# Performance work log

Hardware: AMD Instinct MI355X
Metric: run time of the kernel (lower is better)

## Reference

```python
import jax, jax.numpy as jnp
import numpy as np

U = 256      # lstm_unit / embedding_fc_unit
V = 100000   # word vocab
WD = 300     # word embedding dim
PD = 64      # pos embedding dim
AD = 64      # action embedding dim
P = 50       # pos vocab
NA = 164     # 4 + 4*dep_num actions
B, T, K, L, S, A, DQ = 64, 128, 4, 128, 64, 64, 32
FORGET_BIAS = 1.0


def lstm_step(x, c, h, W, b):
    z = jnp.concatenate([x, h], -1) @ W + b
    i, j, f, o = jnp.split(z, 4, -1)
    nc = c * jax.nn.sigmoid(f + FORGET_BIAS) + jax.nn.sigmoid(i) * jnp.tanh(j)
    nh = jnp.tanh(nc) * jax.nn.sigmoid(o)
    return nc, nh


def run_lstm(xs, length, W, b):
    # xs: [B, L, D]; TF dynamic_rnn semantics: state frozen and output zeroed past length.
    Bn, Ln, _ = xs.shape
    u = W.shape[1] // 4
    def step(carry, tx):
        c, h = carry
        t, x = tx
        nc, nh = lstm_step(x, c, h, W, b)
        m = (t < length)[:, None]
        return (jnp.where(m, nc, c), jnp.where(m, nh, h)), jnp.where(m, nh, 0.0)
    init = (jnp.zeros((Bn, u), xs.dtype), jnp.zeros((Bn, u), xs.dtype))
    (cf, hf), outs = jax.lax.scan(step, init, (jnp.arange(Ln), jnp.swapaxes(xs, 0, 1)))
    return jnp.swapaxes(outs, 0, 1), (cf, hf)


def reverse_seq(xs, length):
    # tf.reverse_sequence: reverse first `length` steps, leave the rest in place.
    Ln = xs.shape[1]
    t = jnp.arange(Ln)[None, :]
    rev = jnp.where(t < length[:, None], length[:, None] - 1 - t, t)
    return jnp.take_along_axis(xs, rev[:, :, None], axis=1)


def forward(tree_word_id, tree_pos_id, token_word_id, token_pos_id, history_action_id,
            buff_top_id, deque_word_id, deque_pos_id, deque_length, children_order,
            stack_order, stack_length, token_length, history_action_length,
            word_emb, pos_emb, act_emb, wd_W, wd_b, tree_W, tree_b,
            stack0_W, stack0_b, stack1_W, stack1_b,
            fw0_W, fw0_b, bw0_W, bw0_b, fw1_W, fw1_b, bw1_W, bw1_b,
            act0_W, act0_b, act1_W, act1_b, dq0_W, dq0_b, dq1_W, dq1_b,
            fin_W, fin_b):
    Bn = tree_word_id.shape[0]

    def embed(wid, pid):
        e = jnp.concatenate([word_emb[wid], pos_emb[pid]], -1)
        return jax.nn.relu(e @ wd_W + wd_b)

    tree_e = embed(tree_word_id, tree_pos_id)       # [B, T, U]
    token_e = embed(token_word_id, token_pos_id)    # [B, L, U]
    deque_e = embed(deque_word_id, deque_pos_id)    # [B, DQ, U]
    hist_e = act_emb[history_action_id]             # [B, A, AD]

    # ---- tree LSTM over children structure ----
    Tn = tree_e.shape[1]
    Kn = children_order.shape[2]
    batch_col = jnp.arange(Bn)[:, None]
    H0 = jnp.zeros((Tn + 1, Bn, U), tree_e.dtype)
    C0 = jnp.zeros((Tn + 1, Bn, U), tree_e.dtype)

    def body(carry, i):
        H, C = carry
        idx = children_order[:, i]            # [B, K] indices into slots 0..i
        h = H[idx, batch_col]                 # [B, K, U]
        c = C[idx, batch_col]
        x = tree_e[:, i]                      # [B, U]
        hj = h.sum(1)
        ijo = jnp.concatenate([x, hj], -1) @ tree_W[:, :3 * U] + tree_b[:3 * U]
        xk = jnp.broadcast_to(x[:, None, :], (Bn, Kn, x.shape[-1]))
        f = jnp.concatenate([xk, h], -1) @ tree_W[:, 3 * U:] + tree_b[3 * U:]   # [B, K, U]
        ig, jg, og = jnp.split(ijo, 3, -1)
        nc = (c * jax.nn.sigmoid(f + FORGET_BIAS)).sum(1) + jax.nn.sigmoid(ig) * jnp.tanh(jg)
        nh = jnp.tanh(nc) * jax.nn.sigmoid(og)
        return (H.at[i + 1].set(nh), C.at[i + 1].set(nc)), None

    (H, _), _ = jax.lax.scan(body, (H0, C0), jnp.arange(Tn))
    stack_embedded = H[stack_order, batch_col]      # [B, S, U]

    # ---- stack LSTM (2-layer) ----
    o0, _ = run_lstm(stack_embedded, stack_length, stack0_W, stack0_b)
    _, (_, stack_h) = run_lstm(o0, stack_length, stack1_W, stack1_b)

    # ---- buff bi-LSTM (2 stacked bidirectional layers) ----
    fw0_o, _ = run_lstm(token_e, token_length, fw0_W, fw0_b)
    bw0_o, _ = run_lstm(reverse_seq(token_e, token_length), token_length, bw0_W, bw0_b)
    bw0_o = reverse_seq(bw0_o, token_length)
    x1 = jnp.concatenate([fw0_o, bw0_o], -1)
    fw1_o, (_, fw1_h) = run_lstm(x1, token_length, fw1_W, fw1_b)
    bw1_o, _ = run_lstm(reverse_seq(x1, token_length), token_length, bw1_W, bw1_b)
    bw1_o = reverse_seq(bw1_o, token_length)
    bidx = jnp.arange(Bn)
    fw_top = fw1_o[bidx, buff_top_id]
    bw_top = bw1_o[bidx, buff_top_id]
    bw_bottom = bw1_o[bidx, token_length - 1]
    buff_out = jnp.concatenate([fw1_h - fw_top, bw_top - bw_bottom], -1)

    # ---- action LSTM (2-layer) ----
    a0, _ = run_lstm(hist_e, history_action_length, act0_W, act0_b)
    _, (_, act_h) = run_lstm(a0, history_action_length, act1_W, act1_b)

    # ---- deque LSTM (2-layer) ----
    d0, _ = run_lstm(deque_e, deque_length, dq0_W, dq0_b)
    _, (_, dq_h) = run_lstm(d0, deque_length, dq1_W, dq1_b)

    feat = jnp.concatenate([stack_h, buff_out, act_h, dq_h], -1)   # [B, 5U]
    return jax.nn.relu(feat @ fin_W + fin_b)


def setup_inputs():
    key = jax.random.key(0)
    ks = jax.random.split(key, 48)
    r = lambda i, shape: jax.random.normal(ks[i], shape, jnp.float32) * 0.05
    ri = lambda i, shape, hi: jax.random.randint(ks[i], shape, 0, hi)
    inp = {}
    inp['tree_word_id'] = ri(0, (B, T), V)
    inp['tree_pos_id'] = ri(1, (B, T), P)
    inp['token_word_id'] = ri(2, (B, L), V)
    inp['token_pos_id'] = ri(3, (B, L), P)
    inp['history_action_id'] = ri(4, (B, A), NA)
    inp['buff_top_id'] = ri(5, (B,), L // 2)
    inp['deque_word_id'] = ri(6, (B, DQ), V)
    inp['deque_pos_id'] = ri(7, (B, DQ), P)
    inp['deque_length'] = jax.random.randint(ks[8], (B,), 1, DQ + 1)
    co = ri(9, (B, T, K), T)
    # a node may only reference already-computed children slots (<= step index)
    inp['children_order'] = jnp.minimum(co, jnp.arange(T)[None, :, None])
    inp['stack_order'] = ri(10, (B, S), T + 1)
    inp['stack_length'] = jax.random.randint(ks[11], (B,), 1, S + 1)
    inp['token_length'] = jax.random.randint(ks[12], (B,), L // 2, L + 1)
    inp['history_action_length'] = jax.random.randint(ks[13], (B,), 1, A + 1)
    inp['word_emb'] = r(14, (V, WD))
    inp['pos_emb'] = r(15, (P, PD))
    inp['act_emb'] = r(16, (NA, AD))
    inp['wd_W'] = r(17, (WD + PD, U)); inp['wd_b'] = jnp.zeros((U,))
    inp['tree_W'] = r(18, (2 * U, 4 * U)); inp['tree_b'] = jnp.zeros((4 * U,))
    inp['stack0_W'] = r(19, (2 * U, 4 * U)); inp['stack0_b'] = jnp.zeros((4 * U,))
    inp['stack1_W'] = r(20, (2 * U, 4 * U)); inp['stack1_b'] = jnp.zeros((4 * U,))
    inp['fw0_W'] = r(21, (2 * U, 4 * U)); inp['fw0_b'] = jnp.zeros((4 * U,))
    inp['bw0_W'] = r(22, (2 * U, 4 * U)); inp['bw0_b'] = jnp.zeros((4 * U,))
    inp['fw1_W'] = r(23, (3 * U, 4 * U)); inp['fw1_b'] = jnp.zeros((4 * U,))
    inp['bw1_W'] = r(24, (3 * U, 4 * U)); inp['bw1_b'] = jnp.zeros((4 * U,))
    inp['act0_W'] = r(25, (AD + U, 4 * U)); inp['act0_b'] = jnp.zeros((4 * U,))
    inp['act1_W'] = r(26, (2 * U, 4 * U)); inp['act1_b'] = jnp.zeros((4 * U,))
    inp['dq0_W'] = r(27, (2 * U, 4 * U)); inp['dq0_b'] = jnp.zeros((4 * U,))
    inp['dq1_W'] = r(28, (2 * U, 4 * U)); inp['dq1_b'] = jnp.zeros((4 * U,))
    inp['fin_W'] = r(29, (5 * U, NA)); inp['fin_b'] = jnp.zeros((NA,))
    return inp


def reference(tree_word_id, tree_pos_id, token_word_id, token_pos_id, history_action_id,
              buff_top_id, deque_word_id, deque_pos_id, deque_length, children_order,
              stack_order, stack_length, token_length, history_action_length,
              word_emb, pos_emb, act_emb, wd_W, wd_b, tree_W, tree_b,
              stack0_W, stack0_b, stack1_W, stack1_b,
              fw0_W, fw0_b, bw0_W, bw0_b, fw1_W, fw1_b, bw1_W, bw1_b,
              act0_W, act0_b, act1_W, act1_b, dq0_W, dq0_b, dq1_W, dq1_b,
              fin_W, fin_b):
    return forward(tree_word_id, tree_pos_id, token_word_id, token_pos_id, history_action_id,
                   buff_top_id, deque_word_id, deque_pos_id, deque_length, children_order,
                   stack_order, stack_length, token_length, history_action_length,
                   word_emb, pos_emb, act_emb, wd_W, wd_b, tree_W, tree_b,
                   stack0_W, stack0_b, stack1_W, stack1_b,
                   fw0_W, fw0_b, bw0_W, bw0_b, fw1_W, fw1_b, bw1_W, bw1_b,
                   act0_W, act0_b, act1_W, act1_b, dq0_W, dq0_b, dq1_W, dq1_b,
                   fin_W, fin_b)
```

## Files before the change

kernel.cpp:

```cpp
#include <hip/hip_runtime.h>
#include <hip/hip_bf16.h>
#include <hip/hip_fp16.h>
#include <cstdint>

#define BB   64
#define TT   128
#define KK   4
#define LL   128
#define SS   64
#define AA   64
#define DQN  32
#define UU   256
#define NAOUT 164
#define WDIM 300
#define PDIM 64
#define ADIM 64

#define OFF_TREE 0
#define OFF_S0   512
#define OFF_S1   1024
#define OFF_FW0  1536
#define OFF_BW0  2048
#define OFF_FW1  2560
#define OFF_BW1  3328
// ... 7 lines not shown
#define PKH_BW0  768
#define PKH_FW1  1024
#define PKH_BW1  1280
#define PKH_S0   1536
#define PKH_S1   1792
#define PKH_ACT0 2048
#define PKH_ACT1 2304
#define PKH_DQ0  2560
#define PKH_DQ1  2816
#define PK_ROWS_B 3072

typedef unsigned short ushort_t;
typedef unsigned int   uint_t;

__device__ __forceinline__ float bf2f(ushort_t s) {
    return __uint_as_float(((uint_t)s) << 16);
}
__device__ __forceinline__ ushort_t f2bf(float x) {
    __hip_bfloat16 h = __float2bfloat16(x);
    return *reinterpret_cast<ushort_t*>(&h);
}
__device__ __forceinline__ float sigm(float x) { return 1.0f / (1.0f + expf(-x)); }

__device__ __forceinline__ uint_t pack2h(float a, float b) {
    __half2 h = __floats2half2_rn(a, b);
    return *reinterpret_cast<uint_t*>(&h);
}
__device__ __forceinline__ float2 unp2h(uint_t v) {
    __half2 h = *reinterpret_cast<__half2*>(&v);
    return __half22float2(h);
}

template<bool F32>
__device__ __forceinline__ float ld1(const void* p_, size_t i) {
    if constexpr (F32) return reinterpret_cast<const float*>(p_)[i];
    else               return bf2f(reinterpret_cast<const ushort_t*>(p_)[i]);
}

struct P {
    const int *tree_word_id, *tree_pos_id, *token_word_id, *token_pos_id, *history_action_id,
              *buff_top_id, *deque_word_id, *deque_pos_id, *deque_length, *children_order,
              *stack_order, *stack_length, *token_length, *history_action_length;
    const void *word_emb, *pos_emb, *act_emb, *wd_W, *wd_b, *tree_W, *tree_b,
        *stack0_W, *stack0_b, *stack1_W, *stack1_b, *fw0_W, *fw0_b, *bw0_W, *bw0_b,
        *fw1_W, *fw1_b, *bw1_W, *bw1_b, *act0_W, *act0_b, *act1_W, *act1_b,
        *dq0_W, *dq0_b, *dq1_W, *dq1_b, *fin_W, *fin_b;
    int* flag;
    float *stack_h, *fw1_h, *fw_top, *bw_top, *bw_bottom, *act_h, *dq_h;
    float *tree_e;
    ushort_t *token_e, *deque_e, *x1;
    float *H, *C;
    float *a0_seq, *d0_seq, *s0_seq;
    uint2 *zxA, *zxB, *zxC, *zxD, *zxS;
    float4* pkf;
};

__global__ void detect_kernel(const uint_t* w, int* flag) {
    __shared__ int cnt;
    if (threadIdx.x == 0) cnt = 0;
    __syncthreads();
    int local = 0;
    for (int i = threadIdx.x; i < 256; i += 64) {
        uint_t lo = w[i] & 0xFFFFu;
        uint_t e  = (lo >> 7) & 0xFFu;
        if (lo == 0u || (e >= 0x6Cu && e <= 0x7Fu)) local++;
    }
    atomicAdd(&cnt, local);
    __syncthreads();
    if (threadIdx.x == 0) flag[0] = (cnt >= 200) ? 0 : 1;
}

__global__ void sentinel_kernel(void* out, float v) {
    if (threadIdx.x == 0) {
        reinterpret_cast<float*>(out)[0] = v;
        reinterpret_cast<__hip_bfloat16*>(out)[2] = __float2bfloat16(v);
    }
}

__global__ __launch_bounds__(256) void pack_fb_kernel(P p) {
    const bool f32 = (p.flag[0] == 1);
    const int rg = blockIdx.x;
    const int u  = threadIdx.x;
    const void* src; int r;
    if      (rg < 512)  { src = p.tree_W;   r = rg; }
    else if (rg < 1024) { src = p.stack0_W; r = rg - 512; }
    else if (rg < 1536) { src = p.stack1_W; r = rg - 1024; }
    else if (rg < 2048) { src = p.fw0_W;    r = rg - 1536; }
    else if (rg < 2560) { src = p.bw0_W;    r = rg - 2048; }
    else if (rg < 3328) { src = p.fw1_W;    r = rg - 2560; }
    else if (rg < 4096) { src = p.bw1_W;    r = rg - 3328; }
    else if (rg < 4416) { src = p.act0_W;   r = rg - 4096; }
    else if (rg < 4928) { src = p.act1_W;   r = rg - 4416; }
    else if (rg < 5440) { src = p.dq0_W;    r = rg - 4928; }
    else                { src = p.dq1_W;    r = rg - 5440; }
    const size_t ro = (size_t)r * 1024;
    float4 v;
    if (f32) {
        const float* s = reinterpret_cast<const float*>(src) + ro;
        v = make_float4(s[u], s[256 + u], s[512 + u], s[768 + u]);
    } else {
        const ushort_t* s = reinterpret_cast<const ushort_t*>(src) + ro;
        v = make_float4(bf2f(s[u]), bf2f(s[256 + u]), bf2f(s[512 + u]), bf2f(s[768 + u]));
    }
    p.pkf[(size_t)rg * 256 + u] = v;
}

// ... 158 lines not shown
                #pragma unroll
                for (int j = 0; j < 4; ++j) {
                    const float4 wv = w[4 * q + j];
                    zi = fmaf(xv[j], wv.x, zi);
                    zj = fmaf(xv[j], wv.y, zj);
                    zo = fmaf(xv[j], wv.z, zo);
                    fx = fmaf(xv[j], wv.w, fx);
                }
            }
        }
        float f0 = 0.f, f1 = 0.f, f2 = 0.f, f3 = 0.f;
        for (int r0 = 0; r0 < 256; r0 += 16) {
            float4 w[16];
            #pragma unroll
            for (int k = 0; k < 16; ++k) w[k] = Wh[(size_t)(r0 + k) * 256];
            __builtin_amdgcn_sched_barrier(0);
            #pragma unroll
            for (int q = 0; q < 4; ++q) {
                const int r = r0 + 4 * q;
                const float4 hj4 = *reinterpret_cast<const float4*>(s_hj + r);
                const float4 a0  = *reinterpret_cast<const float4*>(s_hk + r);
                const float4 a1  = *reinterpret_cast<const float4*>(s_hk + 256 + r);
                const float4 a2  = *reinterpret_cast<const float4*>(s_hk + 512 + r);
                const float4 a3  = *reinterpret_cast<const float4*>(s_hk + 768 + r);
                const float hjv[4] = {hj4.x, hj4.y, hj4.z, hj4.w};
                const float k0[4]  = {a0.x, a0.y, a0.z, a0.w};
                const float k1[4]  = {a1.x, a1.y, a1.z, a1.w};
                const float k2[4]  = {a2.x, a2.y, a2.z, a2.w};
                const float k3[4]  = {a3.x, a3.y, a3.z, a3.w};
                #pragma unroll
                for (int j = 0; j < 4; ++j) {
                    const float4 wv = w[4 * q + j];
                    zi = fmaf(hjv[j], wv.x, zi);
                    zj = fmaf(hjv[j], wv.y, zj);
                    zo = fmaf(hjv[j], wv.z, zo);
                    f0 = fmaf(k0[j], wv.w, f0);
                    f1 = fmaf(k1[j], wv.w, f1);
                    f2 = fmaf(k2[j], wv.w, f2);
                    f3 = fmaf(k3[j], wv.w, f3);
                }
            }
        }
        const float fsum = c0 * sigm(fx + f0) + c1 * sigm(fx + f1)
                         + c2 * sigm(fx + f2) + c3 * sigm(fx + f3);
        const float nc = fsum + sigm(zi) * tanhf(zj);
        const float nh = tanhf(nc) * sigm(zo);
        __syncthreads();
        H[((size_t)(i + 1) * BB + b) * UU + u] = nh;
        C[((size_t)(i + 1) * BB + b) * UU + u] = nc;
    }
}

template<bool F32>
__device__ void run_token_l0_f4(int b, const P& p, float* smem, bool is_bw) {
    const int u = threadIdx.x;
    float* s_xh = smem;
    const int len = p.token_length[b];
    const float4* __restrict__ Wp = p.pkf + (size_t)(is_bw ? OFF_BW0 : OFF_FW0) * 256 + u;
    const float4 bz = load_bias4<F32>(is_bw ? p.bw0_b : p.fw0_b, u);

    float c0 = 0.f;
    s_xh[256 + u] = 0.f;
    for (int t = 0; t < len; ++t) {
        const int row = is_bw ? (len - 1 - t) : t;
        s_xh[u] = bf2f(p.token_e[((size_t)b * LL + row) * UU + u]);
        __syncthreads();
        const float nh = lstm_step_f4<512>(Wp, bz, s_xh, c0);
        p.x1[((size_t)b * LL + row) * 512 + (is_bw ? 256 : 0) + u] = f2bf(nh);
        __syncthreads();
        s_xh[256 + u] = nh;
    }
}

template<bool F32>
__device__ void run_act_dq_f4(int b, const P& p, float* smem) {
    const int u = threadIdx.x;
    float* s_xh0 = smem;
    float* s_xh1 = smem + 512;

    {
        const int len = p.history_action_length[b];
        const float4* __restrict__ W0 = p.pkf + (size_t)OFF_ACT0 * 256 + u;
        const float4* __restrict__ W1 = p.pkf + (size_t)OFF_ACT1 * 256 + u;
        const float4 bz0 = load_bias4<F32>(p.act0_b, u);
        const float4 bz1 = load_bias4<F32>(p.act1_b, u);
        float ca0 = 0.f, ca1 = 0.f, h1last = 0.f;
        s_xh0[ADIM + u] = 0.f;
        s_xh1[256 + u]  = 0.f;
        for (int t = 0; t < len; ++t) {
            const int aid = p.history_action_id[b * AA + t];
            if (u < ADIM) s_xh0[u] = ld1<F32>(p.act_emb, (size_t)aid * ADIM + u);
            __syncthreads();
            const float nh0 = lstm_step_f4<320>(W0, bz0, s_xh0, ca0);
            __syncthreads();
            s_xh0[ADIM + u] = nh0;
            s_xh1[u]        = nh0;
            __syncthreads();
            const float nh1 = lstm_step_f4<512>(W1, bz1, s_xh1, ca1);
            __syncthreads();
            s_xh1[256 + u] = nh1;
            h1last = nh1;
        }
        p.act_h[b * UU + u] = h1last;
    }
    __syncthreads();
    {
// ... 113 lines not shown
    } else {
        if (chain == 0)      run_stack_f4<false>(b, p, smem);
        else if (chain == 1) run_token_l1_f4<false>(b, p, smem, false);
        else                 run_token_l1_f4<false>(b, p, smem, true);
    }
}

template<bool F32, int R>
__device__ void xpre_compute(const void* __restrict__ W, const void* __restrict__ bias,
                             uint2* __restrict__ zx, int n0,
                             const float* __restrict__ s_xf, const ushort_t* __restrict__ s_xb) {
    const int u = threadIdx.x;
    const float4 bz = load_bias4<F32>(bias, u);
    for (int c = 0; c < 32; c += 8) {
        float4 acc[8];
        #pragma unroll
        for (int n = 0; n < 8; ++n) acc[n] = bz;
        for (int r0 = 0; r0 < R; r0 += 8) {
            float4 w[8];
            #pragma unroll
            for (int k = 0; k < 8; ++k) {
                const size_t ro = (size_t)(r0 + k) * 1024;
                w[k] = make_float4(ld1<F32>(W, ro + u),
                                   ld1<F32>(W, ro + 256 + u),
                                   ld1<F32>(W, ro + 512 + u),
                                   ld1<F32>(W, ro + 768 + u));
            }
            #pragma unroll
            for (int n = 0; n < 8; ++n) {
                float xv[8];
                #pragma unroll
                for (int k = 0; k < 8; ++k)
                    xv[k] = (R == 512) ? bf2f(s_xb[(size_t)(c + n) * 512 + r0 + k])
                                       : s_xf[(size_t)(c + n) * R + r0 + k];
                #pragma unroll
                for (int k = 0; k < 8; ++k) {
                    acc[n].x = fmaf(xv[k], w[k].x, acc[n].x);
                    acc[n].y = fmaf(xv[k], w[k].y, acc[n].y);
                    acc[n].z = fmaf(xv[k], w[k].z, acc[n].z);
                    acc[n].w = fmaf(xv[k], w[k].w, acc[n].w);
                }
            }
        }
        #pragma unroll
        for (int n = 0; n < 8; ++n) {
            uint2 v;
            v.x = pack2h(acc[n].x, acc[n].y);
            v.y = pack2h(acc[n].z, acc[n].w);
            zx[(size_t)(n0 + c + n) * 256 + u] = v;
        }
    }
}

template<bool F32, int STAGE>
__device__ void xpre_impl(const P& p, char* s_raw) {
    float*    s_xf = reinterpret_cast<float*>(s_raw);
    ushort_t* s_xb = reinterpret_cast<ushort_t*>(s_raw);
    const int blk = blockIdx.x;
    const int tid = threadIdx.x;

    const void* W; const void* bias; uint2* zx; int R; int kind; int n0;
    if (STAGE == 0) {
        if (blk < 256)      { W=p.fw0_W;  bias=p.fw0_b;  zx=p.zxA; R=256; kind=0; n0=blk*32; }
        else if (blk < 512) { W=p.bw0_W;  bias=p.bw0_b;  zx=p.zxB; R=256; kind=0; n0=(blk-256)*32; }
        else if (blk < 640) { W=p.act0_W; bias=p.act0_b; zx=p.zxC; R=64;  kind=3; n0=(blk-512)*32; }
        else                { W=p.dq0_W;  bias=p.dq0_b;  zx=p.zxD; R=256; kind=1; n0=(blk-640)*32; }
    } else if (STAGE == 1) {
        if (blk < 256)      { W=p.fw1_W;    bias=p.fw1_b;    zx=p.zxA; R=512; kind=2; n0=blk*32; }
        else if (blk < 512) { W=p.bw1_W;    bias=p.bw1_b;    zx=p.zxB; R=512; kind=2; n0=(blk-256)*32; }
        else if (blk < 640) { W=p.stack0_W; bias=p.stack0_b; zx=p.zxS; R=256; kind=4; n0=(blk-512)*32; }
        else if (blk < 768) { W=p.act1_W;   bias=p.act1_b;   zx=p.zxC; R=256; kind=5; n0=(blk-640)*32; }
        else                { W=p.dq1_W;    bias=p.dq1_b;    zx=p.zxD; R=256; kind=6; n0=(blk-768)*32; }
    } else {
        W=p.stack1_W; bias=p.stack1_b; zx=p.zxS; R=256; kind=7; n0=blk*32;
    }

    if (kind == 0 || kind == 1) {
        const ushort_t* src = (kind == 0 ? p.token_e : p.deque_e) + (size_t)n0 * 256;
        for (int i = tid; i < 32 * 256; i += 256) s_xf[i] = bf2f(src[i]);
    } else if (kind == 2) {
        const ushort_t* src = p.x1 + (size_t)n0 * 512;
        for (int i = tid; i < 32 * 512; i += 256) s_xb[i] = src[i];
    } else if (kind == 3) {
        const int b = n0 >> 6, t0 = n0 & 63;
        for (int i = tid; i < 32 * 64; i += 256) {
            const int t = t0 + (i >> 6), r = i & 63;
            int aid = p.history_action_id[b * AA + t];
            aid = aid < 0 ? 0 : (aid > NAOUT - 1 ? NAOUT - 1 : aid);
            s_xf[i] = ld1<F32>(p.act_emb, (size_t)aid * ADIM + r);
        }
    } else if (kind == 4) {
        const int b = n0 >> 6, t0 = n0 & 63;
        for (int i = tid; i < 32 * 256; i += 256) {
            const int t = t0 + (i >> 8), r = i & 255;
            int so = p.stack_order[b * SS + t];
            so = so < 0 ? 0 : (so > TT ? TT : so);
            s_xf[i] = p.H[((size_t)so * BB + b) * UU + r];
        }
    } else {
        const float* src = (kind == 5 ? p.a0_seq : kind == 6 ? p.d0_seq : p.s0_seq)
                         + (size_t)n0 * 256;
        for (int i = tid; i < 32 * 256; i += 256) s_xf[i] = src[i];
    }
    __syncthreads();

    if (R == 512)      xpre_compute<F32, 512>(W, bias, zx, n0, s_xf, s_xb);
    else if (R == 256) xpre_compute<F32, 256>(W, bias, zx, n0, s_xf, s_xb);
    else               xpre_compute<F32, 64 >(W, bias, zx, n0, s_xf, s_xb);
}

__global__ __launch_bounds__(256) void xpre0_kernel(P p) {
    __shared__ __align__(16) char s_raw[32768];
    if (p.flag[0] == 1) xpre_impl<true, 0>(p, s_raw);
    else                xpre_impl<false, 0>(p, s_raw);
}
__global__ __launch_bounds__(256) void xpre1_kernel(P p) {
    __shared__ __align__(16) char s_raw[32768];
    if (p.flag[0] == 1) xpre_impl<true, 1>(p, s_raw);
    else                xpre_impl<false, 1>(p, s_raw);
}
__global__ __launch_bounds__(256) void xpre2_kernel(P p) {
    __shared__ __align__(16) char s_raw[32768];
    if (p.flag[0] == 1) xpre_impl<true, 2>(p, s_raw);
    else                xpre_impl<false, 2>(p, s_raw);
}

template<bool F32>
__device__ void p1_impl(const P& p, float* smem) {
    const int chain = blockIdx.x >> 6;
    const int b     = blockIdx.x & 63;
    if (chain == 0) { run_tree_f4<F32>(b, p, smem); return; }

    const int u = threadIdx.x;
    float* s_h = smem;
    float c = 0.f;
    s_h[u] = 0.f;
    __syncthreads();

    if (chain == 1 || chain == 2) {
        const bool bw = (chain == 2);
        const int len = p.token_length[b];
        const float4* __restrict__ Wh = p.pkf + (size_t)(bw ? PKH_BW0 : PKH_FW0) * 256 + u;
        const uint2* zx = bw ? p.zxB : p.zxA;
        for (int t = 0; t < len; ++t) {
            const int row = bw ? (len - 1 - t) : t;
            const float4 bz = zx_load(zx, (size_t)b * LL + row, u);
            const float nh = lstm_step_f4<256>(Wh, bz, s_h, c);
            p.x1[((size_t)b * LL + row) * 512 + (bw ? 256 : 0) + u] = f2bf(nh);
            __syncthreads();
            s_h[u] = nh;
            __syncthreads();
        }
    } else if (chain == 3) {
        const int len = p.history_action_length[b];
        const float4* __restrict__ Wh = p.pkf + (size_t)PKH_ACT0 * 256 + u;
        for (int t = 0; t < len; ++t) {
            const float4 bz = zx_load(p.zxC, (size_t)b * AA + t, u);
            const float nh = lstm_step_f4<256>(Wh, bz, s_h, c);
            p.a0_seq[((size_t)b * AA + t) * UU + u] = nh;
            __syncthreads();
            s_h[u] = nh;
            __syncthreads();
        }
    } else {
        const int len = p.deque_length[b];
        const float4* __restrict__ Wh = p.pkf + (size_t)PKH_DQ0 * 256 + u;
        for (int t = 0; t < len; ++t) {
            const float4 bz = zx_load(p.zxD, (size_t)b * DQN + t, u);
            const float nh = lstm_step_f4<256>(Wh, bz, s_h, c);
            p.d0_seq[((size_t)b * DQN + t) * UU + u] = nh;
            __syncthreads();
            s_h[u] = nh;
            __syncthreads();
        }
    }
}

__global__ __launch_bounds__(256) void p1_kernel(P p) {
    __shared__ __align__(16) float smem[1536];
    if (p.flag[0] == 1) p1_impl<true>(p, smem);
    else                p1_impl<false>(p, smem);
}

template<bool F32>
__device__ void p2_impl(const P& p, float* smem) {
    const int chain = blockIdx.x >> 6;
    const int b     = blockIdx.x & 63;
    const int u = threadIdx.x;
    float* s_h = smem;
    float c = 0.f;
    s_h[u] = 0.f;
    __syncthreads();

    if (chain == 0) {
        const int len  = p.token_length[b];
        const int btop = p.buff_top_id[b];
        const float4* __restrict__ Wh = p.pkf + (size_t)PKH_FW1 * 256 + u;
        float hlast = 0.f;
        for (int t = 0; t < len; ++t) {
            const float4 bz = zx_load(p.zxA, (size_t)b * LL + t, u);
            const float nh = lstm_step_f4<256>(Wh, bz, s_h, c);
            if (t == btop) p.fw_top[b * UU + u] = nh;
            __syncthreads();
            s_h[u] = nh;
            __syncthreads();
            hlast = nh;
        }
        p.fw1_h[b * UU + u] = hlast;
    } else if (chain == 1) {
        const int len  = p.token_length[b];
        const int btop = p.buff_top_id[b];
        const float4* __restrict__ Wh = p.pkf + (size_t)PKH_BW1 * 256 + u;
        for (int t = 0; t < len; ++t) {
            const int row = len - 1 - t;
            const float4 bz = zx_load(p.zxB, (size_t)b * LL + row, u);
            const float nh = lstm_step_f4<256>(Wh, bz, s_h, c);
            if (t == 0)              p.bw_bottom[b * UU + u] = nh;
            if (t == len - 1 - btop) p.bw_top[b * UU + u]    = nh;
            __syncthreads();
            s_h[u] = nh;
            __syncthreads();
        }
    } else if (chain == 2) {
        const int len = p.stack_length[b];
        const float4* __restrict__ Wh = p.pkf + (size_t)PKH_S0 * 256 + u;
        for (int t = 0; t < len; ++t) {
            const float4 bz = zx_load(p.zxS, (size_t)b * SS + t, u);
            const float nh = lstm_step_f4<256>(Wh, bz, s_h, c);
            p.s0_seq[((size_t)b * SS + t) * UU + u] = nh;
            __syncthreads();
            s_h[u] = nh;
            __syncthreads();
        }
    } else if (chain == 3) {
        const int len = p.history_action_length[b];
        const float4* __restrict__ Wh = p.pkf + (size_t)PKH_ACT1 * 256 + u;
        float hlast = 0.f;
        for (int t = 0; t < len; ++t) {
            const float4 bz = zx_load(p.zxC, (size_t)b * AA + t, u);
            const float nh = lstm_step_f4<256>(Wh, bz, s_h, c);
            __syncthreads();
            s_h[u] = nh;
            __syncthreads();
            hlast = nh;
        }
        p.act_h[b * UU + u] = hlast;
    } else {
        const int len = p.deque_length[b];
        const float4* __restrict__ Wh = p.pkf + (size_t)PKH_DQ1 * 256 + u;
        float hlast = 0.f;
        for (int t = 0; t < len; ++t) {
            const float4 bz = zx_load(p.zxD, (size_t)b * DQN + t, u);
            const float nh = lstm_step_f4<256>(Wh, bz, s_h, c);
            __syncthreads();
            s_h[u] = nh;
            __syncthreads();
            hlast = nh;
        }
        p.dq_h[b * UU + u] = hlast;
    }
}

__global__ __launch_bounds__(256) void p2_kernel(P p) {
    __shared__ __align__(16) float smem[256];
    if (p.flag[0] == 1) p2_impl<true>(p, smem);
    else                p2_impl<false>(p, smem);
}

template<bool F32>
__device__ void p3_impl(const P& p, float* smem) {
    const int b = blockIdx.x;
    const int u = threadIdx.x;
    float* s_h = smem;
    float c = 0.f;
    s_h[u] = 0.f;
    __syncthreads();
    const int len = p.stack_length[b];
    const float4* __restrict__ Wh = p.pkf + (size_t)PKH_S1 * 256 + u;
    float hlast = 0.f;
    for (int t = 0; t < len; ++t) {
        const float4 bz = zx_load(p.zxS, (size_t)b * SS + t, u);
        const float nh = lstm_step_f4<256>(Wh, bz, s_h, c);
        __syncthreads();
        s_h[u] = nh;
        __syncthreads();
        hlast = nh;
    }
    p.stack_h[b * UU + u] = hlast;
}

__global__ __launch_bounds__(256) void p3_kernel(P p) {
    __shared__ __align__(16) float smem[256];
    if (p.flag[0] == 1) p3_impl<true>(p, smem);
    else                p3_impl<false>(p, smem);
}

template<bool F32>
__device__ __forceinline__ void st_out(void* out, int i, float v) {
    if constexpr (F32) reinterpret_cast<float*>(out)[i] = v;
    else               reinterpret_cast<__hip_bfloat16*>(out)[i] = __float2bfloat16(v);
}

template<bool F32>
__device__ void final_impl(const P& p, void* out, float* s_f) {
    const int b = blockIdx.x;
    const int u = threadIdx.x;
    s_f[u]        = p.stack_h[b * UU + u];
    s_f[256 + u]  = p.fw1_h[b * UU + u] - p.fw_top[b * UU + u];
    s_f[512 + u]  = p.bw_top[b * UU + u] - p.bw_bottom[b * UU + u];
    s_f[768 + u]  = p.act_h[b * UU + u];
    s_f[1024 + u] = p.dq_h[b * UU + u];
    __syncthreads();
    if (u < NAOUT) {
        float acc = ld1<F32>(p.fin_b, u);
        for (int r = 0; r < 1280; ++r)
            acc = fmaf(s_f[r], ld1<F32>(p.fin_W, (size_t)r * NAOUT + u), acc);
        acc = fmaxf(acc, 0.f);
        st_out<F32>(out, b * NAOUT + u, acc);
    }
    if (b == 0 && u == 0) {
        const uint_t POIS = 0xAAAAAAAAu;
        const uint_t* te = reinterpret_cast<const uint_t*>(p.tree_e);
        const uint_t* x1 = reinterpret_cast<const uint_t*>(p.x1);
        const uint_t* sh = reinterpret_cast<const uint_t*>(p.stack_h);
        bool te_p = true, x1_p = true;
        for (int i = 0; i < 8; ++i) { te_p &= (te[i] == POIS); x1_p &= (x1[i] == POIS); }
        bool sh_p = (sh[0] == POIS) && (sh[1] == POIS);
        float sent = 0.f;
        if (te_p)      sent = 3000.f;
        else if (x1_p) sent = 4000.f;
        else if (sh_p) sent = 5000.f;
        else if (*reinterpret_cast<const uint_t*>(p.flag) == POIS) sent = 6000.f;
        if (sent > 0.f) st_out<F32>(out, 0, sent);
    }
}

__global__ __launch_bounds__(256) void final_kernel(P p, void* out) {
// ... 36 lines not shown
    p.wd_b     = d_in[18];
    p.tree_W   = d_in[19];
    p.tree_b   = d_in[20];
    p.stack0_W = d_in[21];
    p.stack0_b = d_in[22];
    p.stack1_W = d_in[23];
    p.stack1_b = d_in[24];
    p.fw0_W    = d_in[25];
    p.fw0_b    = d_in[26];
    p.bw0_W    = d_in[27];
    p.bw0_b    = d_in[28];
    p.fw1_W    = d_in[29];
    p.fw1_b    = d_in[30];
    p.bw1_W    = d_in[31];
    p.bw1_b    = d_in[32];
    p.act0_W   = d_in[33];
    p.act0_b   = d_in[34];
    p.act1_W   = d_in[35];
    p.act1_b   = d_in[36];
    p.dq0_W    = d_in[37];
    p.dq0_b    = d_in[38];
    p.dq1_W    = d_in[39];
    p.dq1_b    = d_in[40];
    p.fin_W    = d_in[41];
    p.fin_b    = d_in[42];

    char* base = (char*)d_ws;

    size_t off = 0;
    p.flag = (int*)(base + off);           off += 256;
    p.stack_h   = (float*)(base + off);    off += (size_t)BB * UU * 4;
    p.fw1_h     = (float*)(base + off);    off += (size_t)BB * UU * 4;
    p.fw_top    = (float*)(base + off);    off += (size_t)BB * UU * 4;
    p.bw_top    = (float*)(base + off);    off += (size_t)BB * UU * 4;
    p.bw_bottom = (float*)(base + off);    off += (size_t)BB * UU * 4;
    p.act_h     = (float*)(base + off);    off += (size_t)BB * UU * 4;
    p.dq_h      = (float*)(base + off);    off += (size_t)BB * UU * 4;
    p.tree_e  = (float*)(base + off);      off += (size_t)BB * TT * UU * 4;
    p.token_e = (ushort_t*)(base + off);   off += (size_t)BB * LL * UU * 2;
    p.deque_e = (ushort_t*)(base + off);   off += (size_t)BB * DQN * UU * 2;
    p.x1      = (ushort_t*)(base + off);   off += (size_t)BB * LL * 512 * 2;
    p.a0_seq  = (float*)(base + off);      off += (size_t)BB * AA * UU * 4;
    p.d0_seq  = (float*)(base + off);      off += (size_t)BB * DQN * UU * 4;
    p.s0_seq  = (float*)(base + off);      off += (size_t)BB * SS * UU * 4;
    p.H       = (float*)(base + off);      off += (size_t)(TT + 1) * BB * UU * 4;
    p.C       = (float*)(base + off);      off += (size_t)(TT + 1) * BB * UU * 4;
    p.zxA     = (uint2*)(base + off);      off += (size_t)BB * LL * UU * 8;
    p.zxB     = (uint2*)(base + off);      off += (size_t)BB * LL * UU * 8;
    p.zxC     = (uint2*)(base + off);      off += (size_t)BB * AA * UU * 8;
    p.zxD     = (uint2*)(base + off);      off += (size_t)BB * DQN * UU * 8;
    p.zxS     = (uint2*)(base + off);      off += (size_t)BB * SS * UU * 8;
    p.pkf     = (float4*)(base + off);     off += (size_t)PK_ROWS_B * 256 * 16;
    const size_t planB_size = off;

    if (ws_size >= planB_size) {
        detect_kernel<<<1, 64, 0, stream>>>((const uint_t*)d_in[14], p.flag);
        pack_h_kernel<<<dim3(PK_ROWS_B), dim3(256), 0, stream>>>(p);
        embed_kernel<<<dim3(BB * TT + BB * LL + BB * DQN), dim3(256), 0, stream>>>(p);
        xpre0_kernel<<<dim3(704), dim3(256), 0, stream>>>(p);
        p1_kernel<<<dim3(5 * BB), dim3(256), 0, stream>>>(p);
        xpre1_kernel<<<dim3(832), dim3(256), 0, stream>>>(p);
        p2_kernel<<<dim3(5 * BB), dim3(256), 0, stream>>>(p);
        xpre2_kernel<<<dim3(128), dim3(256), 0, stream>>>(p);
        p3_kernel<<<dim3(BB), dim3(256), 0, stream>>>(p);
        final_kernel<<<dim3(BB), dim3(256), 0, stream>>>(p, d_out);
        return;
    }

    off = 0;
    p.flag = (int*)(base + off);           off += 16;
    p.stack_h   = (float*)(base + off);    off += (size_t)BB * UU * 4;
    p.fw1_h     = (float*)(base + off);    off += (size_t)BB * UU * 4;
    p.fw_top    = (float*)(base + off);    off += (size_t)BB * UU * 4;
    p.bw_top    = (float*)(base + off);    off += (size_t)BB * UU * 4;
    p.bw_bottom = (float*)(base + off);    off += (size_t)BB * UU * 4;
    p.act_h     = (float*)(base + off);    off += (size_t)BB * UU * 4;
    p.dq_h      = (float*)(base + off);    off += (size_t)BB * UU * 4;
    p.tree_e  = (float*)(base + off);      off += (size_t)BB * TT * UU * 4;
    p.token_e = (ushort_t*)(base + off);   off += (size_t)BB * LL * UU * 2;
    p.deque_e = (ushort_t*)(base + off);   off += (size_t)BB * DQN * UU * 2;
    p.x1      = (ushort_t*)(base + off);   off += (size_t)BB * LL * 512 * 2;
    p.H       = (float*)(base + off);      off += (size_t)(TT + 1) * BB * UU * 4;
    p.C       = (float*)(base + off);      off += (size_t)(TT + 1) * BB * UU * 4;
    p.pkf     = (float4*)(base + off);     off += (size_t)PK_ROWS_FB * 256 * 16;
    p.a0_seq = p.d0_seq = p.s0_seq = (float*)base;
    p.zxA = p.zxB = p.zxC = p.zxD = p.zxS = (uint2*)base;

    if (ws_size < off) {
        sentinel_kernel<<<1, 64, 0, stream>>>(d_out, 7000.f + (float)(ws_size >> 20));
        return;
    }

    detect_kernel<<<1, 64, 0, stream>>>((const uint_t*)d_in[14], p.flag);
    pack_fb_kernel<<<dim3(PK_ROWS_FB), dim3(256), 0, stream>>>(p);
    embed_kernel<<<dim3(BB * TT + BB * LL + BB * DQN), dim3(256), 0, stream>>>(p);
    phase1_fb_kernel<<<dim3(4 * BB), dim3(256), 0, stream>>>(p);
    phase2_fb_kernel<<<dim3(3 * BB), dim3(256), 0, stream>>>(p);
    final_kernel<<<dim3(BB), dim3(256), 0, stream>>>(p, d_out);
}
```

Baseline: 6.336 ms.

## Precompute tree input projections and interleave recurrent chains across CUs

Adds a tree-LSTM input-projection stage to the batched pre-GEMM kernel, writing fp32 float4 gates into a new workspace buffer. The tree recurrence then only does the hidden-state matmul per step, which shortens the serial critical path. The recurrent phases are also remapped so that long chains (tree, token, stack) are spread across the block index with short chains interleaved, which is meant to balance load across CUs. The cost is a larger workspace requirement, an extra 32MB buffer, and idle blocks that exit early.

```diff
diff --git a/kernel.cpp b/kernel.cpp
--- a/kernel.cpp
+++ b/kernel.cpp
@@ -83,6 +83,7 @@
     float *H, *C;
     float *a0_seq, *d0_seq, *s0_seq;
     uint2 *zxA, *zxB, *zxC, *zxD, *zxS;
+    float4* zxT;
     float4* pkf;
 };
 
@@ -347,6 +348,79 @@
 }
 
 template<bool F32>
+__device__ void run_tree_hc(int b, const P& p, float* smem) {
+    const int u = threadIdx.x;
+    float* s_hj = smem;
+    float* s_hk = smem + 256;
+    float* H = p.H;
+    float* C = p.C;
+    H[(size_t)b * UU + u] = 0.f;
+    C[(size_t)b * UU + u] = 0.f;
+    const float4* __restrict__ Wh = p.pkf + (size_t)256 * 256 + u;
+
+    for (int i = 0; i < TT; ++i) {
+        const int* co = p.children_order + ((size_t)b * TT + i) * KK;
+        const int i0 = co[0], i1 = co[1], i2 = co[2], i3 = co[3];
+        const float h0 = H[((size_t)i0 * BB + b) * UU + u];
+        const float h1 = H[((size_t)i1 * BB + b) * UU + u];
+        const float h2 = H[((size_t)i2 * BB + b) * UU + u];
+        const float h3 = H[((size_t)i3 * BB + b) * UU + u];
+        const float c0 = C[((size_t)i0 * BB + b) * UU + u];
+        const float c1 = C[((size_t)i1 * BB + b) * UU + u];
+        const float c2 = C[((size_t)i2 * BB + b) * UU + u];
+        const float c3 = C[((size_t)i3 * BB + b) * UU + u];
+        s_hk[u]       = h0;
+        s_hk[256 + u] = h1;
+        s_hk[512 + u] = h2;
+        s_hk[768 + u] = h3;
+        s_hj[u]       = h0 + h1 + h2 + h3;
+        __syncthreads();
+
+        const float4 z0 = p.zxT[((size_t)b * TT + i) * 256 + u];
+        float zi = z0.x, zj = z0.y, zo = z0.z, fx = z0.w;
+        float f0 = 0.f, f1 = 0.f, f2 = 0.f, f3 = 0.f;
+        for (int r0 = 0; r0 < 256; r0 += 16) {
+            float4 w[16];
+            #pragma unroll
+            for (int k = 0; k < 16; ++k) w[k] = Wh[(size_t)(r0 + k) * 256];
+            __builtin_amdgcn_sched_barrier(0);
+            #pragma unroll
+            for (int q = 0; q < 4; ++q) {
+                const int r = r0 + 4 * q;
+                const float4 hj4 = *reinterpret_cast<const float4*>(s_hj + r);
+                const float4 a0  = *reinterpret_cast<const float4*>(s_hk + r);
+                const float4 a1  = *reinterpret_cast<const float4*>(s_hk + 256 + r);
+                const float4 a2  = *reinterpret_cast<const float4*>(s_hk + 512 + r);
+                const float4 a3  = *reinterpret_cast<const float4*>(s_hk + 768 + r);
+                const float hjv[4] = {hj4.x, hj4.y, hj4.z, hj4.w};
+                const float k0[4]  = {a0.x, a0.y, a0.z, a0.w};
+                const float k1[4]  = {a1.x, a1.y, a1.z, a1.w};
+                const float k2[4]  = {a2.x, a2.y, a2.z, a2.w};
+                const float k3[4]  = {a3.x, a3.y, a3.z, a3.w};
+                #pragma unroll
+                for (int j = 0; j < 4; ++j) {
+                    const float4 wv = w[4 * q + j];
+                    zi = fmaf(hjv[j], wv.x, zi);
+                    zj = fmaf(hjv[j], wv.y, zj);
+                    zo = fmaf(hjv[j], wv.z, zo);
+                    f0 = fmaf(k0[j], wv.w, f0);
+                    f1 = fmaf(k1[j], wv.w, f1);
+                    f2 = fmaf(k2[j], wv.w, f2);
+                    f3 = fmaf(k3[j], wv.w, f3);
+                }
+            }
+        }
+        const float fsum = c0 * sigm(fx + f0) + c1 * sigm(fx + f1)
+                         + c2 * sigm(fx + f2) + c3 * sigm(fx + f3);
+        const float nc = fsum + sigm(zi) * tanhf(zj);
+        const float nh = tanhf(nc) * sigm(zo);
+        __syncthreads();
+        H[((size_t)(i + 1) * BB + b) * UU + u] = nh;
+        C[((size_t)(i + 1) * BB + b) * UU + u] = nc;
+    }
+}
+
+template<bool F32>
 __device__ void run_token_l0_f4(int b, const P& p, float* smem, bool is_bw) {
     const int u = threadIdx.x;
     float* s_xh = smem;
@@ -566,6 +640,46 @@
     }
 }
 
+template<bool F32>
+__device__ void xpre_tree_compute(const void* __restrict__ W, const void* __restrict__ bias,
+                                  float4* __restrict__ zxT, int n0,
+                                  const float* __restrict__ s_xf) {
+    const int u = threadIdx.x;
+    const float4 bz = make_float4(ld1<F32>(bias, u), ld1<F32>(bias, 256 + u),
+                                  ld1<F32>(bias, 512 + u),
+                                  ld1<F32>(bias, 768 + u) + 1.0f);
+    for (int c = 0; c < 32; c += 8) {
+        float4 acc[8];
+        #pragma unroll
+        for (int n = 0; n < 8; ++n) acc[n] = bz;
+        for (int r0 = 0; r0 < 256; r0 += 8) {
+            float4 w[8];
+            #pragma unroll
+            for (int k = 0; k < 8; ++k) {
+                const size_t ro = (size_t)(r0 + k) * 1024;
+                w[k] = make_float4(ld1<F32>(W, ro + u),
+                                   ld1<F32>(W, ro + 256 + u),
+                                   ld1<F32>(W, ro + 512 + u),
+                                   ld1<F32>(W, ro + 768 + u));
+            }
+            #pragma unroll
+            for (int n = 0; n < 8; ++n) {
+                #pragma unroll
+                for (int k = 0; k < 8; ++k) {
+                    const float xv = s_xf[(size_t)(c + n) * 256 + r0 + k];
+                    acc[n].x = fmaf(xv, w[k].x, acc[n].x);
+                    acc[n].y = fmaf(xv, w[k].y, acc[n].y);
+                    acc[n].z = fmaf(xv, w[k].z, acc[n].z);
+                    acc[n].w = fmaf(xv, w[k].w, acc[n].w);
+                }
+            }
+        }
+        #pragma unroll
+        for (int n = 0; n < 8; ++n)
+            zxT[(size_t)(n0 + c + n) * 256 + u] = acc[n];
+    }
+}
+
 template<bool F32, int STAGE>
 __device__ void xpre_impl(const P& p, char* s_raw) {
     float*    s_xf = reinterpret_cast<float*>(s_raw);
@@ -573,12 +687,13 @@
     const int blk = blockIdx.x;
     const int tid = threadIdx.x;
 
-    const void* W; const void* bias; uint2* zx; int R; int kind; int n0;
+    const void* W; const void* bias; uint2* zx = nullptr; int R; int kind; int n0;
     if (STAGE == 0) {
         if (blk < 256)      { W=p.fw0_W;  bias=p.fw0_b;  zx=p.zxA; R=256; kind=0; n0=blk*32; }
         else if (blk < 512) { W=p.bw0_W;  bias=p.bw0_b;  zx=p.zxB; R=256; kind=0; n0=(blk-256)*32; }
         else if (blk < 640) { W=p.act0_W; bias=p.act0_b; zx=p.zxC; R=64;  kind=3; n0=(blk-512)*32; }
-        else                { W=p.dq0_W;  bias=p.dq0_b;  zx=p.zxD; R=256; kind=1; n0=(blk-640)*32; }
+        else if (blk < 704) { W=p.dq0_W;  bias=p.dq0_b;  zx=p.zxD; R=256; kind=1; n0=(blk-640)*32; }
+        else                { W=p.tree_W; bias=p.tree_b; R=256;    kind=8; n0=(blk-704)*32; }
     } else if (STAGE == 1) {
         if (blk < 256)      { W=p.fw1_W;    bias=p.fw1_b;    zx=p.zxA; R=512; kind=2; n0=blk*32; }
         else if (blk < 512) { W=p.bw1_W;    bias=p.bw1_b;    zx=p.zxB; R=512; kind=2; n0=(blk-256)*32; }
@@ -611,6 +726,9 @@
             so = so < 0 ? 0 : (so > TT ? TT : so);
             s_xf[i] = p.H[((size_t)so * BB + b) * UU + r];
         }
+    } else if (kind == 8) {
+        const float* src = p.tree_e + (size_t)n0 * 256;
+        for (int i = tid; i < 32 * 256; i += 256) s_xf[i] = src[i];
     } else {
         const float* src = (kind == 5 ? p.a0_seq : kind == 6 ? p.d0_seq : p.s0_seq)
                          + (size_t)n0 * 256;
@@ -618,7 +736,8 @@
     }
     __syncthreads();
 
-    if (R == 512)      xpre_compute<F32, 512>(W, bias, zx, n0, s_xf, s_xb);
+    if (kind == 8)     xpre_tree_compute<F32>(W, bias, p.zxT, n0, s_xf);
+    else if (R == 512) xpre_compute<F32, 512>(W, bias, zx, n0, s_xf, s_xb);
     else if (R == 256) xpre_compute<F32, 256>(W, bias, zx, n0, s_xf, s_xb);
     else               xpre_compute<F32, 64 >(W, bias, zx, n0, s_xf, s_xb);
 }
@@ -640,163 +759,259 @@
 }
 
 template<bool F32>
-__device__ void p1_impl(const P& p, float* smem) {
-    const int chain = blockIdx.x >> 6;
-    const int b     = blockIdx.x & 63;
-    if (chain == 0) { run_tree_f4<F32>(b, p, smem); return; }
-
-    const int u = threadIdx.x;
-    float* s_h = smem;
+__device__ void chain_token_l0(int b, const P& p, float* s_h, bool bw) {
+    const int u = threadIdx.x;
+    const int len = p.token_length[b];
+    const float4* __restrict__ Wh = p.pkf + (size_t)(bw ? PKH_BW0 : PKH_FW0) * 256 + u;
+    const uint2* zx = bw ? p.zxB : p.zxA;
     float c = 0.f;
     s_h[u] = 0.f;
     __syncthreads();
-
-    if (chain == 1 || chain == 2) {
-        const bool bw = (chain == 2);
-        const int len = p.token_length[b];
-        const float4* __restrict__ Wh = p.pkf + (size_t)(bw ? PKH_BW0 : PKH_FW0) * 256 + u;
-        const uint2* zx = bw ? p.zxB : p.zxA;
-        for (int t = 0; t < len; ++t) {
-            const int row = bw ? (len - 1 - t) : t;
-            const float4 bz = zx_load(zx, (size_t)b * LL + row, u);
-            const float nh = lstm_step_f4<256>(Wh, bz, s_h, c);
-            p.x1[((size_t)b * LL + row) * 512 + (bw ? 256 : 0) + u] = f2bf(nh);
-            __syncthreads();
-            s_h[u] = nh;
-            __syncthreads();
-        }
-    } else if (chain == 3) {
-        const int len = p.history_action_length[b];
-        const float4* __restrict__ Wh = p.pkf + (size_t)PKH_ACT0 * 256 + u;
-        for (int t = 0; t < len; ++t) {
-            const float4 bz = zx_load(p.zxC, (size_t)b * AA + t, u);
-            const float nh = lstm_step_f4<256>(Wh, bz, s_h, c);
-            p.a0_seq[((size_t)b * AA + t) * UU + u] = nh;
-            __syncthreads();
-            s_h[u] = nh;
-            __syncthreads();
-        }
-    } else {
-        const int len = p.deque_length[b];
-        const float4* __restrict__ Wh = p.pkf + (size_t)PKH_DQ0 * 256 + u;
-        for (int t = 0; t < len; ++t) {
-            const float4 bz = zx_load(p.zxD, (size_t)b * DQN + t, u);
-            const float nh = lstm_step_f4<256>(Wh, bz, s_h, c);
-            p.d0_seq[((size_t)b * DQN + t) * UU + u] = nh;
-            __syncthreads();
-            s_h[u] = nh;
-            __syncthreads();
-        }
-    }
-}
-
-__global__ __launch_bounds__(256) void p1_kernel(P p) {
-    __shared__ __align__(16) float smem[1536];
-    if (p.flag[0] == 1) p1_impl<true>(p, smem);
-    else                p1_impl<false>(p, smem);
-}
-
-template<bool F32>
-__device__ void p2_impl(const P& p, float* smem) {
-    const int chain = blockIdx.x >> 6;
-    const int b     = blockIdx.x & 63;
-    const int u = threadIdx.x;
-    float* s_h = smem;
+    for (int t = 0; t < len; ++t) {
+        const int row = bw ? (len - 1 - t) : t;
+        const float4 bz = zx_load(zx, (size_t)b * LL + row, u);
+        const float nh = lstm_step_f4<256>(Wh, bz, s_h, c);
+        p.x1[((size_t)b * LL + row) * 512 + (bw ? 256 : 0) + u] = f2bf(nh);
+        __syncthreads();
+        s_h[u] = nh;
+        __syncthreads();
+    }
+}
+
+template<bool F32>
+__device__ void chain_act0(int b, const P& p, float* s_h) {
+    const int u = threadIdx.x;
+    const int len = p.history_action_length[b];
+    const float4* __restrict__ Wh = p.pkf + (size_t)PKH_ACT0 * 256 + u;
     float c = 0.f;
     s_h[u] = 0.f;
     __syncthreads();
-
-    if (chain == 0) {
-        const int len  = p.token_length[b];
-        const int btop = p.buff_top_id[b];
-        const float4* __restrict__ Wh = p.pkf + (size_t)PKH_FW1 * 256 + u;
-        float hlast = 0.f;
-        for (int t = 0; t < len; ++t) {
-            const float4 bz = zx_load(p.zxA, (size_t)b * LL + t, u);
-            const float nh = lstm_step_f4<256>(Wh, bz, s_h, c);
-            if (t == btop) p.fw_top[b * UU + u] = nh;
-            __syncthreads();
-            s_h[u] = nh;
-            __syncthreads();
-            hlast = nh;
-        }
-        p.fw1_h[b * UU + u] = hlast;
-    } else if (chain == 1) {
-        const int len  = p.token_length[b];
-        const int btop = p.buff_top_id[b];
-        const float4* __restrict__ Wh = p.pkf + (size_t)PKH_BW1 * 256 + u;
-        for (int t = 0; t < len; ++t) {
-            const int row = len - 1 - t;
-            const float4 bz = zx_load(p.zxB, (size_t)b * LL + row, u);
-            const float nh = lstm_step_f4<256>(Wh, bz, s_h, c);
-            if (t == 0)              p.bw_bottom[b * UU + u] = nh;
-            if (t == len - 1 - btop) p.bw_top[b * UU + u]    = nh;
-            __syncthreads();
-            s_h[u] = nh;
-            __syncthreads();
-        }
-    } else if (chain == 2) {
-        const int len = p.stack_length[b];
-        const float4* __restrict__ Wh = p.pkf + (size_t)PKH_S0 * 256 + u;
-        for (int t = 0; t < len; ++t) {
-            const float4 bz = zx_load(p.zxS, (size_t)b * SS + t, u);
-            const float nh = lstm_step_f4<256>(Wh, bz, s_h, c);
-            p.s0_seq[((size_t)b * SS + t) * UU + u] = nh;
-            __syncthreads();
-            s_h[u] = nh;
-            __syncthreads();
-        }
-    } else if (chain == 3) {
-        const int len = p.history_action_length[b];
-        const float4* __restrict__ Wh = p.pkf + (size_t)PKH_ACT1 * 256 + u;
-        float hlast = 0.f;
-        for (int t = 0; t < len; ++t) {
-            const float4 bz = zx_load(p.zxC, (size_t)b * AA + t, u);
-            const float nh = lstm_step_f4<256>(Wh, bz, s_h, c);
-            __syncthreads();
-            s_h[u] = nh;
-            __syncthreads();
-            hlast = nh;
-        }
-        p.act_h[b * UU + u] = hlast;
-    } else {
-        const int len = p.deque_length[b];
-        const float4* __restrict__ Wh = p.pkf + (size_t)PKH_DQ1 * 256 + u;
-        float hlast = 0.f;
-        for (int t = 0; t < len; ++t) {
-            const float4 bz = zx_load(p.zxD, (size_t)b * DQN + t, u);
-            const float nh = lstm_step_f4<256>(Wh, bz, s_h, c);
-            __syncthreads();
-            s_h[u] = nh;
-            __syncthreads();
-            hlast = nh;
-        }
-        p.dq_h[b * UU + u] = hlast;
-    }
-}
-
-__global__ __launch_bounds__(256) void p2_kernel(P p) {
-    __shared__ __align__(16) float smem[256];
-    if (p.flag[0] == 1) p2_impl<true>(p, smem);
-    else                p2_impl<false>(p, smem);
-}
-
-template<bool F32>
-__device__ void p3_impl(const P& p, float* smem) {
-    const int b = blockIdx.x;
-    const int u = threadIdx.x;
-    float* s_h = smem;
+    for (int t = 0; t < len; ++t) {
+        const float4 bz = zx_load(p.zxC, (size_t)b * AA + t, u);
+        const float nh = lstm_step_f4<256>(Wh, bz, s_h, c);
+        p.a0_seq[((size_t)b * AA + t) * UU + u] = nh;
+        __syncthreads();
+        s_h[u] = nh;
+        __syncthreads();
+    }
+}
+
+template<bool F32>
+__device__ void chain_dq0(int b, const P& p, float* s_h) {
+    const int u = threadIdx.x;
+    const int len = p.deque_length[b];
+    const float4* __restrict__ Wh = p.pkf + (size_t)PKH_DQ0 * 256 + u;
     float c = 0.f;
     s_h[u] = 0.f;
     __syncthreads();
+    for (int t = 0; t < len; ++t) {
+        const float4 bz = zx_load(p.zxD, (size_t)b * DQN + t, u);
+        const float nh = lstm_step_f4<256>(Wh, bz, s_h, c);
+        p.d0_seq[((size_t)b * DQN + t) * UU + u] = nh;
+        __syncthreads();
+        s_h[u] = nh;
+        __syncthreads();
+    }
+}
+
+template<bool F32>
+__device__ void chain_fw1(int b, const P& p, float* s_h) {
+    const int u = threadIdx.x;
+    const int len  = p.token_length[b];
+    const int btop = p.buff_top_id[b];
+    const float4* __restrict__ Wh = p.pkf + (size_t)PKH_FW1 * 256 + u;
+    float c = 0.f, hlast = 0.f;
+    s_h[u] = 0.f;
+    __syncthreads();
+    for (int t = 0; t < len; ++t) {
+        const float4 bz = zx_load(p.zxA, (size_t)b * LL + t, u);
+        const float nh = lstm_step_f4<256>(Wh, bz, s_h, c);
+        if (t == btop) p.fw_top[b * UU + u] = nh;
+        __syncthreads();
+        s_h[u] = nh;
+        __syncthreads();
+        hlast = nh;
+    }
+    p.fw1_h[b * UU + u] = hlast;
+}
+
+template<bool F32>
+__device__ void chain_bw1(int b, const P& p, float* s_h) {
+    const int u = threadIdx.x;
+    const int len  = p.token_length[b];
+    const int btop = p.buff_top_id[b];
+    const float4* __restrict__ Wh = p.pkf + (size_t)PKH_BW1 * 256 + u;
+    float c = 0.f;
+    s_h[u] = 0.f;
+    __syncthreads();
+    for (int t = 0; t < len; ++t) {
+        const int row = len - 1 - t;
+        const float4 bz = zx_load(p.zxB, (size_t)b * LL + row, u);
+        const float nh = lstm_step_f4<256>(Wh, bz, s_h, c);
+        if (t == 0)              p.bw_bottom[b * UU + u] = nh;
+        if (t == len - 1 - btop) p.bw_top[b * UU + u]    = nh;
+        __syncthreads();
+        s_h[u] = nh;
+        __syncthreads();
+    }
+}
+
+template<bool F32>
+__device__ void chain_stack0(int b, const P& p, float* s_h) {
+    const int u = threadIdx.x;
     const int len = p.stack_length[b];
-    const float4* __restrict__ Wh = p.pkf + (size_t)PKH_S1 * 256 + u;
-    float hlast = 0.f;
+    const float4* __restrict__ Wh = p.pkf + (size_t)PKH_S0 * 256 + u;
+    float c = 0.f;
+    s_h[u] = 0.f;
+    __syncthreads();
     for (int t = 0; t < len; ++t) {
         const float4 bz = zx_load(p.zxS, (size_t)b * SS + t, u);
         const float nh = lstm_step_f4<256>(Wh, bz, s_h, c);
+        p.s0_seq[((size_t)b * SS + t) * UU + u] = nh;
         __syncthreads();
         s_h[u] = nh;
+        __syncthreads();
+    }
+}
+
+template<bool F32>
+__device__ void chain_act1(int b, const P& p, float* s_h) {
+    const int u = threadIdx.x;
+    const int len = p.history_action_length[b];
+    const float4* __restrict__ Wh = p.pkf + (size_t)PKH_ACT1 * 256 + u;
+    float c = 0.f, hlast = 0.f;
+    s_h[u] = 0.f;
+    __syncthreads();
+    for (int t = 0; t < len; ++t) {
+        const float4 bz = zx_load(p.zxC, (size_t)b * AA + t, u);
+        const float nh = lstm_step_f4<256>(Wh, bz, s_h, c);
+        __syncthreads();
+        s_h[u] = nh;
+        __syncthreads();
+        hlast = nh;
+    }
+    p.act_h[b * UU + u] = hlast;
+}
+
+template<bool F32>
+__device__ void chain_dq1(int b, const P& p, float* s_h) {
+    const int u = threadIdx.x;
+    const int len = p.deque_length[b];
+    const float4* __restrict__ Wh = p.pkf + (size_t)PKH_DQ1 * 256 + u;
+    float c = 0.f, hlast = 0.f;
+    s_h[u] = 0.f;
+    __syncthreads();
+    for (int t = 0; t < len; ++t) {
+        const float4 bz = zx_load(p.zxD, (size_t)b * DQN + t, u);
+        const float nh = lstm_step_f4<256>(Wh, bz, s_h, c);
+        __syncthreads();
+        s_h[u] = nh;
+        __syncthreads();
+        hlast = nh;
+    }
+    p.dq_h[b * UU + u] = hlast;
+}
+
+template<bool F32>
+__device__ void p1b_impl(const P& p, float* smem) {
+    const int chain = blockIdx.x >> 6;
+    const int b     = blockIdx.x & 63;
+    if (chain == 0)      run_tree_f4<F32>(b, p, smem);
+    else if (chain == 1) chain_token_l0<F32>(b, p, smem, false);
+    else if (chain == 2) chain_token_l0<F32>(b, p, smem, true);
+    else if (chain == 3) chain_act0<F32>(b, p, smem);
+    else                 chain_dq0<F32>(b, p, smem);
+}
+
+__global__ __launch_bounds__(256) void p1b_kernel(P p) {
+    __shared__ __align__(16) float smem[1536];
+    if (p.flag[0] == 1) p1b_impl<true>(p, smem);
+    else                p1b_impl<false>(p, smem);
+}
+
+template<bool F32>
+__device__ void p2b_impl(const P& p, float* smem) {
+    const int chain = blockIdx.x >> 6;
+    const int b     = blockIdx.x & 63;
+    if (chain == 0)      chain_fw1<F32>(b, p, smem);
+    else if (chain == 1) chain_bw1<F32>(b, p, smem);
+    else if (chain == 2) chain_stack0<F32>(b, p, smem);
+    else if (chain == 3) chain_act1<F32>(b, p, smem);
+    else                 chain_dq1<F32>(b, p, smem);
+}
+
+__global__ __launch_bounds__(256) void p2b_kernel(P p) {
+    __shared__ __align__(16) float smem[256];
+    if (p.flag[0] == 1) p2b_impl<true>(p, smem);
+    else                p2b_impl<false>(p, smem);
+}
+
+template<bool F32>
+__device__ void p1c_impl(const P& p, float* smem) {
+    const int s = blockIdx.x & 7;
+    const int j = blockIdx.x >> 3;
+    if (s == 0 || s == 5) {
+        if (j >= 32) return;
+        run_tree_hc<F32>((s == 5 ? 32 : 0) + j, p, smem);
+    } else if (s == 1 || s == 6) {
+        if (j >= 32) return;
+        chain_token_l0<F32>((s == 6 ? 32 : 0) + j, p, smem, false);
+    } else if (s == 2 || s == 7) {
+        if (j >= 32) return;
+        chain_token_l0<F32>((s == 7 ? 32 : 0) + j, p, smem, true);
+    } else if (s == 3) {
+        chain_act0<F32>(j, p, smem);
+    } else {
+        chain_dq0<F32>(j, p, smem);
+    }
+}
+
+__global__ __launch_bounds__(256) void p1c_kernel(P p) {
+    __shared__ __align__(16) float smem[1280];
+    if (p.flag[0] == 1) p1c_impl<true>(p, smem);
+    else                p1c_impl<false>(p, smem);
+}
+
+template<bool F32>
+__device__ void p2c_impl(const P& p, float* smem) {
+    const int s = blockIdx.x & 7;
+    const int j = blockIdx.x >> 3;
+    if (s == 0 || s == 5) {
+        if (j >= 32) return;
+        chain_fw1<F32>((s == 5 ? 32 : 0) + j, p, smem);
+    } else if (s == 1 || s == 6) {
+        if (j >= 32) return;
+        chain_bw1<F32>((s == 6 ? 32 : 0) + j, p, smem);
+    } else if (s == 2 || s == 7) {
+        if (j >= 32) return;
+        chain_stack0<F32>((s == 7 ? 32 : 0) + j, p, smem);
+    } else if (s == 3) {
+        chain_act1<F32>(j, p, smem);
+    } else {
+        chain_dq1<F32>(j, p, smem);
+    }
+}
+
+__global__ __launch_bounds__(256) void p2c_kernel(P p) {
+    __shared__ __align__(16) float smem[256];
+    if (p.flag[0] == 1) p2c_impl<true>(p, smem);
+    else                p2c_impl<false>(p, smem);
+}
+
+template<bool F32>
+__device__ void p3_impl(const P& p, float* smem) {
+    const int b = blockIdx.x;
+    const int u = threadIdx.x;
+    const int len = p.stack_length[b];
+    const float4* __restrict__ Wh = p.pkf + (size_t)PKH_S1 * 256 + u;
+    float c = 0.f, hlast = 0.f;
+    smem[u] = 0.f;
+    __syncthreads();
+    for (int t = 0; t < len; ++t) {
+        const float4 bz = zx_load(p.zxS, (size_t)b * SS + t, u);
+        const float nh = lstm_step_f4<256>(Wh, bz, smem, c);
+        __syncthreads();
+        smem[u] = nh;
         __syncthreads();
         hlast = nh;
     }
@@ -939,15 +1154,32 @@
     p.zxS     = (uint2*)(base + off);      off += (size_t)BB * SS * UU * 8;
     p.pkf     = (float4*)(base + off);     off += (size_t)PK_ROWS_B * 256 * 16;
     const size_t planB_size = off;
+    p.zxT     = (float4*)(base + off);     off += (size_t)BB * TT * UU * 16;
+    const size_t planC_size = off;
+
+    if (ws_size >= planC_size) {
+        detect_kernel<<<1, 64, 0, stream>>>((const uint_t*)d_in[14], p.flag);
+        pack_h_kernel<<<dim3(PK_ROWS_B), dim3(256), 0, stream>>>(p);
+        embed_kernel<<<dim3(BB * TT + BB * LL + BB * DQN), dim3(256), 0, stream>>>(p);
+        xpre0_kernel<<<dim3(960), dim3(256), 0, stream>>>(p);
+        p1c_kernel<<<dim3(512), dim3(256), 0, stream>>>(p);
+        xpre1_kernel<<<dim3(832), dim3(256), 0, stream>>>(p);
+        p2c_kernel<<<dim3(512), dim3(256), 0, stream>>>(p);
+        xpre2_kernel<<<dim3(128), dim3(256), 0, stream>>>(p);
+        p3_kernel<<<dim3(BB), dim3(256), 0, stream>>>(p);
+        final_kernel<<<dim3(BB), dim3(256), 0, stream>>>(p, d_out);
+        return;
+    }
 
     if (ws_size >= planB_size) {
+        p.zxT = (float4*)base;
         detect_kernel<<<1, 64, 0, stream>>>((const uint_t*)d_in[14], p.flag);
         pack_h_kernel<<<dim3(PK_ROWS_B), dim3(256), 0, stream>>>(p);
         embed_kernel<<<dim3(BB * TT + BB * LL + BB * DQN), dim3(256), 0, stream>>>(p);
         xpre0_kernel<<<dim3(704), dim3(256), 0, stream>>>(p);
-        p1_kernel<<<dim3(5 * BB), dim3(256), 0, stream>>>(p);
+        p1b_kernel<<<dim3(5 * BB), dim3(256), 0, stream>>>(p);
         xpre1_kernel<<<dim3(832), dim3(256), 0, stream>>>(p);
-        p2_kernel<<<dim3(5 * BB), dim3(256), 0, stream>>>(p);
+        p2b_kernel<<<dim3(5 * BB), dim3(256), 0, stream>>>(p);
         xpre2_kernel<<<dim3(128), dim3(256), 0, stream>>>(p);
         p3_kernel<<<dim3(BB), dim3(256), 0, stream>>>(p);
         final_kernel<<<dim3(BB), dim3(256), 0, stream>>>(p, d_out);
@@ -972,6 +1204,7 @@
     p.pkf     = (float4*)(base + off);     off += (size_t)PK_ROWS_FB * 256 * 16;
     p.a0_seq = p.d0_seq = p.s0_seq = (float*)base;
     p.zxA = p.zxB = p.zxC = p.zxD = p.zxS = (uint2*)base;
+    p.zxT = (float4*)base;
 
     if (ws_size < off) {
         sentinel_kernel<<<1, 64, 0, stream>>>(d_out, 7000.f + (float)(ws_size >> 20));
```

Result: faster. 5.103 ms (-19.4%).
